# Kernel optimization log

Hardware: AMD Instinct MI355X
Metric: run time of the kernel (lower is better)

## Reference

```python
import jax, jax.numpy as jnp
import numpy as np

N, E, B = 100000, 500000, 64
H, C = 2, 128  # GAT heads, per-head channels
EPS = 1e-5


def _seg_mean(x, idx, n):
    s = jax.ops.segment_sum(x, idx, num_segments=n)
    cnt = jax.ops.segment_sum(jnp.ones((idx.shape[0],), x.dtype), idx, num_segments=n)
    cnt = jnp.maximum(cnt, 1.0)
    return s / cnt.reshape((n,) + (1,) * (x.ndim - 1))


def _bn(x, g, b):
    m = x.mean(0)
    v = x.var(0)  # biased, as torch BN uses for normalization
    return g * (x - m) / jnp.sqrt(v + EPS) + b


def _sage(x, src, dst, n, wl, wr, b):
    # PyG SAGEConv(mean): lin_l(mean_j x_j) + lin_r(x_i), bias on lin_l
    agg = _seg_mean(x[src], dst, n)
    return agg @ wl.T + x @ wr.T + b


def setup_inputs():
    key = jax.random.key(0)
    ks = jax.random.split(key, 24)
    w = lambda k, s: (jax.random.normal(k, s, jnp.float32) * 0.05)
    inp = {
        'pos': jax.random.normal(ks[0], (N, 3), jnp.float32),
        'edge_index': jax.random.randint(ks[1], (2, E), 0, N),
        'batch': jnp.sort(jax.random.randint(ks[2], (N,), 0, B)),
        # SAGEConv 1: 3 -> 128
        's1_wl': w(ks[3], (128, 3)), 's1_wr': w(ks[4], (128, 3)), 's1_b': jnp.zeros((128,), jnp.float32),
        # SAGEConv 2: 128 -> 128
        's2_wl': w(ks[5], (128, 128)), 's2_wr': w(ks[6], (128, 128)), 's2_b': jnp.zeros((128,), jnp.float32),
        # GATConv: 256 -> 128, heads=2, concat=False
        'g_w': w(ks[7], (H * C, 256)), 'g_asrc': w(ks[8], (H, C)), 'g_adst': w(ks[9], (H, C)), 'g_b': jnp.zeros((C,), jnp.float32),
        # decoder
        'd1_w': w(ks[10], (256, 128)), 'd1_b': jnp.zeros((256,), jnp.float32),
        'bn1_g': jnp.ones((256,), jnp.float32), 'bn1_b': jnp.zeros((256,), jnp.float32),
        'd2_w': w(ks[11], (128, 256)), 'd2_b': jnp.zeros((128,), jnp.float32),
        'bn2_g': jnp.ones((128,), jnp.float32), 'bn2_b': jnp.zeros((128,), jnp.float32),
        'd3_w': w(ks[12], (40, 128)), 'd3_b': jnp.zeros((40,), jnp.float32),
        'bn3_g': jnp.ones((40,), jnp.float32), 'bn3_b': jnp.zeros((40,), jnp.float32),
    }
    return inp


def reference(pos, edge_index, batch, s1_wl, s1_wr, s1_b, s2_wl, s2_wr, s2_b,
              g_w, g_asrc, g_adst, g_b, d1_w, d1_b, bn1_g, bn1_b,
              d2_w, d2_b, bn2_g, bn2_b, d3_w, d3_b, bn3_g, bn3_b):
    src, dst = edge_index[0], edge_index[1]

    x1 = jax.nn.relu(_sage(pos, src, dst, N, s1_wl, s1_wr, s1_b))
    x2 = jax.nn.relu(_sage(x1, src, dst, N, s2_wl, s2_wr, s2_b))
    x3 = jnp.concatenate([x1, x2], axis=-1)  # [N, 256]

    # GATConv with self-loops, dropout off (eval), aggr='mean'
    loop = jnp.arange(N, dtype=edge_index.dtype)
    src_sl = jnp.concatenate([src, loop])
    dst_sl = jnp.concatenate([dst, loop])
    xw = (x3 @ g_w.T).reshape(N, H, C)
    a_src = (xw * g_asrc).sum(-1)  # [N, H]
    a_dst = (xw * g_adst).sum(-1)
    e = jax.nn.leaky_relu(a_src[src_sl] + a_dst[dst_sl], 0.2)  # [E+N, H]
    e_max = jax.ops.segment_max(e, dst_sl, num_segments=N)
    e = jnp.exp(e - e_max[dst_sl])
    denom = jax.ops.segment_sum(e, dst_sl, num_segments=N)
    alpha = e / denom[dst_sl]
    msg = alpha[:, :, None] * xw[src_sl]  # [E+N, H, C]
    out = _seg_mean(msg, dst_sl, N)  # aggr='mean' over incoming edges
    x3 = out.mean(axis=1) + g_b  # average heads (concat=False) -> [N, 128]

    z = _seg_mean(x3, batch, B)  # global mean pool -> [B, 128]

    z = jax.nn.relu(_bn(z @ d1_w.T + d1_b, bn1_g, bn1_b))
    z = jax.nn.relu(_bn(z @ d2_w.T + d2_b, bn2_g, bn2_b))
    z = _bn(z @ d3_w.T + d3_b, bn3_g, bn3_b)
    return z, jnp.argmax(z, axis=-1)
```

## Files before the change

kernel.cpp:

```cpp
#include <hip/hip_runtime.h>
#include <math.h>

#define BN_EPS 1e-5f

typedef __attribute__((ext_vector_type(8))) short short8;
typedef __attribute__((ext_vector_type(4))) float f32x4;

__device__ __forceinline__ float bf2f(unsigned short u) {
  return __builtin_bit_cast(float, ((unsigned)u) << 16);
}
__device__ __forceinline__ unsigned short f2bf(float f) {
  unsigned u = __builtin_bit_cast(unsigned, f);
  unsigned r = (u + 0x7fffu + ((u >> 16) & 1u)) >> 16;
  return (unsigned short)r;
}
__device__ __forceinline__ void fsplit(float x, unsigned short& h, unsigned short& l) {
  h = f2bf(x);
  l = f2bf(x - bf2f(h));
}

__global__ void k_deg_sum1(const int* __restrict__ src, const int* __restrict__ dst,
                           const float* __restrict__ pos, int* __restrict__ deg,
                           float* __restrict__ sum1, int E) {
  int e = blockIdx.x * blockDim.x + threadIdx.x;
  if (e >= E) return;
  int s = src[e], d = dst[e];
  atomicAdd(&deg[d], 1);
  atomicAdd(&sum1[d * 3 + 0], pos[s * 3 + 0]);
  atomicAdd(&sum1[d * 3 + 1], pos[s * 3 + 1]);
  atomicAdd(&sum1[d * 3 + 2], pos[s * 3 + 2]);
}

__global__ void k_scan1(const int* __restrict__ deg, int* __restrict__ rowptr,
                        int* __restrict__ bsum, int N) {
  __shared__ int part[256];
  int t = threadIdx.x;
  int base = blockIdx.x * 1024;
  int v[4]; int s = 0;
#pragma unroll
  for (int i = 0; i < 4; i++) {
    int idx = base + t * 4 + i;
    v[i] = (idx < N) ? deg[idx] : 0;
    s += v[i];
  }
  part[t] = s;
  __syncthreads();
  for (int off = 1; off < 256; off <<= 1) {
    int x = (t >= off) ? part[t - off] : 0;
    __syncthreads();
    part[t] += x;
    __syncthreads();
  }
  int run = part[t] - s;
#pragma unroll
  for (int i = 0; i < 4; i++) {
    int idx = base + t * 4 + i;
    if (idx < N) rowptr[idx] = run;
    run += v[i];
  }
  if (t == 255) bsum[blockIdx.x] = part[255];
}

__global__ void k_scan2(int* __restrict__ bsum, int nb) {
  if (threadIdx.x == 0 && blockIdx.x == 0) {
    int run = 0;
    for (int i = 0; i < nb; i++) { int v = bsum[i]; bsum[i] = run; run += v; }
  }
}

__global__ void k_scan3(int* __restrict__ rowptr, const int* __restrict__ bsum,
                        int N, int E) {
  int i = blockIdx.x * blockDim.x + threadIdx.x;
  if (i < N) rowptr[i] += bsum[i >> 10];
  else if (i == N) rowptr[N] = E;
}

__global__ void k_fill(const int* __restrict__ src, const int* __restrict__ dst,
                       const int* __restrict__ rowptr, int* __restrict__ fill,
                       int* __restrict__ col, int E) {
  int e = blockIdx.x * blockDim.x + threadIdx.x;
  if (e >= E) return;
  int d = dst[e];
  int p = rowptr[d] + atomicAdd(&fill[d], 1);
  col[p] = src[e];
}

__global__ void k_sage1(const float* __restrict__ sum1, const int* __restrict__ deg,
                        const float* __restrict__ pos,
                        const float* __restrict__ wl, const float* __restrict__ wr,
                        const float* __restrict__ b,
                        unsigned short* __restrict__ catH, unsigned short* __restrict__ catL,
                        int N) {
  int n = blockIdx.x;
  if (n >= N) return;
  int o = threadIdx.x;
  float c = fmaxf((float)deg[n], 1.f);
  float a0 = sum1[n * 3 + 0] / c, a1 = sum1[n * 3 + 1] / c, a2 = sum1[n * 3 + 2] / c;
  float p0 = pos[n * 3 + 0], p1 = pos[n * 3 + 1], p2 = pos[n * 3 + 2];
  float v = b[o] + wl[o * 3 + 0] * a0 + wl[o * 3 + 1] * a1 + wl[o * 3 + 2] * a2
                 + wr[o * 3 + 0] * p0 + wr[o * 3 + 1] * p1 + wr[o * 3 + 2] * p2;
  v = fmaxf(v, 0.f);
  unsigned short h, l;
  fsplit(v, h, l);
  catH[(size_t)n * 256 + o] = h;
  catL[(size_t)n * 256 + o] = l;
}

__global__ void k_agg_x1(const int* __restrict__ rowptr, const int* __restrict__ col,
                         const unsigned short* __restrict__ catH,
                         const unsigned short* __restrict__ catL,
                         unsigned short* __restrict__ aggH,
                         unsigned short* __restrict__ aggL, int N) {
  int w = (blockIdx.x * blockDim.x + threadIdx.x) >> 6;
  int nw = (gridDim.x * blockDim.x) >> 6;
  int lane = threadIdx.x & 63;
  for (int n = w; n < N; n += nw) {
    int k0 = rowptr[n], k1 = rowptr[n + 1];
    float ax = 0.f, ay = 0.f;
    int k = k0;
    for (; k + 1 < k1; k += 2) {
      int s0 = col[k], s1 = col[k + 1];
      size_t b0 = (size_t)s0 * 256 + lane * 2;
      size_t b1 = (size_t)s1 * 256 + lane * 2;
      ushort2 h0 = *(const ushort2*)&catH[b0];
      ushort2 l0 = *(const ushort2*)&catL[b0];
      ushort2 h1 = *(const ushort2*)&catH[b1];
      ushort2 l1 = *(const ushort2*)&catL[b1];
      ax += (bf2f(h0.x) + bf2f(l0.x)) + (bf2f(h1.x) + bf2f(l1.x));
      ay += (bf2f(h0.y) + bf2f(l0.y)) + (bf2f(h1.y) + bf2f(l1.y));
    }
    if (k < k1) {
      int s = col[k];
      size_t b0 = (size_t)s * 256 + lane * 2;
      ushort2 vh = *(const ushort2*)&catH[b0];
      ushort2 vl = *(const ushort2*)&catL[b0];
      ax += bf2f(vh.x) + bf2f(vl.x);
      ay += bf2f(vh.y) + bf2f(vl.y);
    }
    float inv = 1.f / fmaxf((float)(k1 - k0), 1.f);
    unsigned short hx, lx, hy, ly;
    fsplit(ax * inv, hx, lx);
    fsplit(ay * inv, hy, ly);
    *(ushort2*)&aggH[(size_t)n * 128 + lane * 2] = make_ushort2(hx, hy);
    *(ushort2*)&aggL[(size_t)n * 128 + lane * 2] = make_ushort2(lx, ly);
  }
}

__global__ void k_castcat(const float* __restrict__ a, const float* __restrict__ b,
                          unsigned short* __restrict__ oH, unsigned short* __restrict__ oL,
                          int K1, int K2, int M) {
  int i = blockIdx.x * blockDim.x + threadIdx.x;
  int K = K1 + K2;
  if (i >= M * K) return;
  int m = i / K, k = i - m * K;
  float v = (k < K1) ? a[m * K1 + k] : b[m * K2 + (k - K1)];
  unsigned short h, l;
  fsplit(v, h, l);
  oH[i] = h;
  oL[i] = l;
}

__global__ __launch_bounds__(256) void gemm_split(
    const unsigned short* __restrict__ AH1, const unsigned short* __restrict__ AL1,
    int as1, int K1,
    const unsigned short* __restrict__ AH2, const unsigned short* __restrict__ AL2,
    int as2,
    const unsigned short* __restrict__ WH, const unsigned short* __restrict__ WL,
    const float* __restrict__ bias,
    unsigned short* __restrict__ CH, unsigned short* __restrict__ CL,
    int cs, int co, int Nr, int K, int relu,
    const float* __restrict__ asrc, const float* __restrict__ adst,
    float* __restrict__ attn) {
  __shared__ unsigned short AsH[128][40];
  __shared__ unsigned short AsL[128][40];
  __shared__ unsigned short BsH[128][40];
  __shared__ unsigned short BsL[128][40];
  int tid = threadIdx.x;
  int bm = blockIdx.x, bn = blockIdx.y;
  int wv = tid >> 6, L = tid & 63;
  int m16 = L & 15, quad = L >> 4;
  int rbase = wv * 32;

  f32x4 acc[2][8];
#pragma unroll
  for (int i = 0; i < 2; i++)
#pragma unroll
    for (int j = 0; j < 8; j++) acc[i][j] = (f32x4){0.f, 0.f, 0.f, 0.f};

  for (int kt = 0; kt < K; kt += 32) {
    const unsigned short *ApH, *ApL;
    int ast, kl;
    if (kt < K1) { ApH = AH1; ApL = AL1; ast = as1; kl = kt; }
    else         { ApH = AH2; ApL = AL2; ast = as2; kl = kt - K1; }
#pragma unroll
    for (int i = 0; i < 2; i++) {
      int flat = tid * 2 + i;
      int row = flat >> 2;
      int kc = (flat & 3) * 8;
      int rg = bm * 128 + row;
      uint4 vah = {0u, 0u, 0u, 0u}, val = {0u, 0u, 0u, 0u};
      if (rg < Nr) {
        size_t a = (size_t)rg * ast + kl + kc;
        vah = *(const uint4*)&ApH[a];
        val = *(const uint4*)&ApL[a];
      }
      *(uint4*)&AsH[row][kc] = vah;
      *(uint4*)&AsL[row][kc] = val;
      int ng = bn * 128 + row;
      size_t wb = (size_t)ng * K + kt + kc;
      *(uint4*)&BsH[row][kc] = *(const uint4*)&WH[wb];
      *(uint4*)&BsL[row][kc] = *(const uint4*)&WL[wb];
    }
    __syncthreads();
    short8 afH[2], afL[2];
#pragma unroll
    for (int rt = 0; rt < 2; rt++) {
      afH[rt] = *(const short8*)&AsH[rbase + rt * 16 + m16][quad * 8];
      afL[rt] = *(const short8*)&AsL[rbase + rt * 16 + m16][quad * 8];
    }
#pragma unroll
    for (int ct = 0; ct < 8; ct++) {
      short8 bfH = *(const short8*)&BsH[ct * 16 + m16][quad * 8];
      short8 bfL = *(const short8*)&BsL[ct * 16 + m16][quad * 8];
#pragma unroll
      for (int rt = 0; rt < 2; rt++) {
        acc[rt][ct] = __builtin_amdgcn_mfma_f32_16x16x32_bf16(afH[rt], bfH, acc[rt][ct], 0, 0, 0);
        acc[rt][ct] = __builtin_amdgcn_mfma_f32_16x16x32_bf16(afH[rt], bfL, acc[rt][ct], 0, 0, 0);
        acc[rt][ct] = __builtin_amdgcn_mfma_f32_16x16x32_bf16(afL[rt], bfH, acc[rt][ct], 0, 0, 0);
      }
    }
    __syncthreads();
  }

  const bool doattn = (attn != nullptr);
  float sa[2][4], sd[2][4];
#pragma unroll
  for (int rt = 0; rt < 2; rt++)
#pragma unroll
    for (int r = 0; r < 4; r++) { sa[rt][r] = 0.f; sd[rt][r] = 0.f; }

#pragma unroll
  for (int rt = 0; rt < 2; rt++) {
#pragma unroll
    for (int r = 0; r < 4; r++) {
      int rg = bm * 128 + rbase + rt * 16 + quad * 4 + r;
      if (rg >= Nr) continue;
#pragma unroll
      for (int ct = 0; ct < 8; ct++) {
        int cg = bn * 128 + ct * 16 + m16;
        float v = acc[rt][ct][r];
        if (doattn) {
          sa[rt][r] += v * asrc[cg];
          sd[rt][r] += v * adst[cg];
        }
        if (bias) v += bias[cg];
        if (relu) v = fmaxf(v, 0.f);
        unsigned short h, l;
        fsplit(v, h, l);
        size_t o = (size_t)rg * cs + co + cg;
        CH[o] = h;
        CL[o] = l;
      }
    }
  }

  if (doattn) {
#pragma unroll
    for (int rt = 0; rt < 2; rt++) {
#pragma unroll
      for (int r = 0; r < 4; r++) {
        float a = sa[rt][r], d = sd[rt][r];
#pragma unroll
        for (int m = 8; m >= 1; m >>= 1) {
          a += __shfl_xor(a, m);
          d += __shfl_xor(d, m);
        }
        if (m16 == 0) {
          int rg = bm * 128 + rbase + rt * 16 + quad * 4 + r;
          if (rg < Nr) {
            attn[rg * 4 + bn] = a;
            attn[rg * 4 + 2 + bn] = d;
          }
        }
      }
    }
  }
}

__global__ void k_gat_gather(const int* __restrict__ rowptr, const int* __restrict__ col,
                             const unsigned short* __restrict__ xwH,
                             const unsigned short* __restrict__ xwL,
                             const float* __restrict__ attn,
                             const float* __restrict__ gb, float* __restrict__ x3g, int N) {
  int w = (blockIdx.x * blockDim.x + threadIdx.x) >> 6;
  int nw = (gridDim.x * blockDim.x) >> 6;
  int lane = threadIdx.x & 63;
  int h = lane >> 5;
  for (int n = w; n < N; n += nw) {
    int k0 = rowptr[n], k1 = rowptr[n + 1];
    float ad = attn[n * 4 + 2 + h];
    float a0 = 0.f, a1 = 0.f, a2 = 0.f, a3 = 0.f, den = 0.f;
    int k = k0;
    for (; k + 1 < k1; k += 2) {
      int s0 = col[k], s1 = col[k + 1];
      float e0 = attn[s0 * 4 + h] + ad;
      float e1 = attn[s1 * 4 + h] + ad;
      e0 = e0 >= 0.f ? e0 : 0.2f * e0;
      e1 = e1 >= 0.f ? e1 : 0.2f * e1;
      float w0 = expf(e0), w1 = expf(e1);
      size_t b0 = (size_t)s0 * 256 + lane * 4;
      size_t b1 = (size_t)s1 * 256 + lane * 4;
      ushort4 h0 = *(const ushort4*)&xwH[b0];
      ushort4 l0 = *(const ushort4*)&xwL[b0];
      ushort4 h1 = *(const ushort4*)&xwH[b1];
      ushort4 l1 = *(const ushort4*)&xwL[b1];
      a0 += w0 * (bf2f(h0.x) + bf2f(l0.x)) + w1 * (bf2f(h1.x) + bf2f(l1.x));
      a1 += w0 * (bf2f(h0.y) + bf2f(l0.y)) + w1 * (bf2f(h1.y) + bf2f(l1.y));
      a2 += w0 * (bf2f(h0.z) + bf2f(l0.z)) + w1 * (bf2f(h1.z) + bf2f(l1.z));
      a3 += w0 * (bf2f(h0.w) + bf2f(l0.w)) + w1 * (bf2f(h1.w) + bf2f(l1.w));
      den += w0 + w1;
    }
    if (k < k1) {
      int s = col[k];
      float ea = attn[s * 4 + h] + ad;
      float el = ea >= 0.f ? ea : 0.2f * ea;
      float wgt = expf(el);
      size_t base = (size_t)s * 256 + lane * 4;
      ushort4 xh = *(const ushort4*)&xwH[base];
      ushort4 xl = *(const ushort4*)&xwL[base];
      a0 += wgt * (bf2f(xh.x) + bf2f(xl.x));
      a1 += wgt * (bf2f(xh.y) + bf2f(xl.y));
      a2 += wgt * (bf2f(xh.z) + bf2f(xl.z));
      a3 += wgt * (bf2f(xh.w) + bf2f(xl.w));
      den += wgt;
    }
    {
      float ea = attn[n * 4 + h] + ad;
      float el = ea >= 0.f ? ea : 0.2f * ea;
      float wgt = expf(el);
      size_t base = (size_t)n * 256 + lane * 4;
      ushort4 xh = *(const ushort4*)&xwH[base];
      ushort4 xl = *(const ushort4*)&xwL[base];
      a0 += wgt * (bf2f(xh.x) + bf2f(xl.x));
      a1 += wgt * (bf2f(xh.y) + bf2f(xl.y));
      a2 += wgt * (bf2f(xh.z) + bf2f(xl.z));
      a3 += wgt * (bf2f(xh.w) + bf2f(xl.w));
      den += wgt;
    }
    float invD = 1.f / den;
    float q0 = a0 * invD, q1 = a1 * invD, q2 = a2 * invD, q3 = a3 * invD;
    float p0 = __shfl_xor(q0, 32), p1 = __shfl_xor(q1, 32);
    float p2 = __shfl_xor(q2, 32), p3 = __shfl_xor(q3, 32);
    if (lane < 32) {
      float invc = 1.f / (float)(k1 - k0 + 1);
      float4 g = *(const float4*)&gb[lane * 4];
      float4 r;
      r.x = 0.5f * (q0 + p0) * invc + g.x;
      r.y = 0.5f * (q1 + p1) * invc + g.y;
      r.z = 0.5f * (q2 + p2) * invc + g.z;
      r.w = 0.5f * (q3 + p3) * invc + g.w;
      *(float4*)&x3g[(size_t)n * 128 + lane * 4] = r;
    }
  }
}

__global__ void k_pool(const float* __restrict__ x3g, const int* __restrict__ batch,
                       float* __restrict__ zsum, float* __restrict__ zcnt, int N) {
  int t = threadIdx.x;
  int chunk = (N + gridDim.x - 1) / gridDim.x;
  int n0 = blockIdx.x * chunk;
  int n1 = min(N, n0 + chunk);
  if (n0 >= n1) return;
  int cur = batch[n0];
  float acc = 0.f, cacc = 0.f;
  for (int n = n0; n < n1; n++) {
    int b = batch[n];
    if (b != cur) {
      atomicAdd(&zsum[cur * 128 + t], acc);
      if (t == 0) atomicAdd(&zcnt[cur], cacc);
      acc = 0.f; cacc = 0.f; cur = b;
    }
    acc += x3g[(size_t)n * 128 + t];
    cacc += 1.f;
  }
  atomicAdd(&zsum[cur * 128 + t], acc);
  if (t == 0) atomicAdd(&zcnt[cur], cacc);
}

__global__ void dec_col(const float* __restrict__ X, float* __restrict__ Y,
                        const float* __restrict__ W, const float* __restrict__ bias,
                        const float* __restrict__ g, const float* __restrict__ beta,
                        int Ki, int Mo, int Bn, int relu,
                        const float* __restrict__ zcntp) {
  int m = blockIdx.x;
  int r = threadIdx.x;
  float dot = 0.f;
  const float* xr = &X[(size_t)r * Ki];
  const float* wr = &W[(size_t)m * Ki];
  for (int k = 0; k < Ki; k += 4) {
    float4 xv = *(const float4*)&xr[k];
    float4 wv = *(const float4*)&wr[k];
    dot += xv.x * wv.x + xv.y * wv.y + xv.z * wv.z + xv.w * wv.w;
  }
  if (zcntp) dot *= 1.f / fmaxf(zcntp[r], 1.f);
  float acc = dot + bias[m];
  float s = acc;
#pragma unroll
  for (int o = 32; o >= 1; o >>= 1) s += __shfl_xor(s, o);
  float mean = s / (float)Bn;
  float d = acc - mean;
  float v2 = d * d;
#pragma unroll
  for (int o = 32; o >= 1; o >>= 1) v2 += __shfl_xor(v2, o);
  float var = v2 / (float)Bn;
  float y = g[m] * d / sqrtf(var + BN_EPS) + beta[m];
  if (relu) y = fmaxf(y, 0.f);
  Y[(size_t)r * Mo + m] = y;
}

__global__ void k_argmax(const float* __restrict__ z, float* __restrict__ argout,
                         int Bn, int Mo) {
  int r = blockIdx.x * blockDim.x + threadIdx.x;
  if (r >= Bn) return;
  const float* yr = &z[(size_t)r * Mo];
  float best = yr[0];
  int bi = 0;
  for (int j = 1; j < Mo; j++)
    if (yr[j] > best) { best = yr[j]; bi = j; }
  argout[r] = (float)bi;
}

extern "C" void kernel_launch(void* const* d_in, const int* in_sizes, int n_in,
                              void* d_out, int out_size, void* d_ws, size_t ws_size,
                              hipStream_t stream) {
  const int N = in_sizes[0] / 3;
  const int E = in_sizes[1] / 2;
  const int Bn = out_size / 41;

  const float* pos = (const float*)d_in[0];
  const int* ei = (const int*)d_in[1];
  const int* src = ei;
  const int* dst = ei + E;
  const int* batch = (const int*)d_in[2];
  const float* s1_wl = (const float*)d_in[3];
  const float* s1_wr = (const float*)d_in[4];
  const float* s1_b  = (const float*)d_in[5];
  const float* s2_wl = (const float*)d_in[6];
  const float* s2_wr = (const float*)d_in[7];
  const float* s2_b  = (const float*)d_in[8];
  const float* g_w    = (const float*)d_in[9];
  const float* g_asrc = (const float*)d_in[10];
  const float* g_adst = (const float*)d_in[11];
  const float* g_b    = (const float*)d_in[12];
  const float* d1_w = (const float*)d_in[13];
  const float* d1_b = (const float*)d_in[14];
  const float* bn1_g = (const float*)d_in[15];
  const float* bn1_b = (const float*)d_in[16];
  const float* d2_w = (const float*)d_in[17];
  const float* d2_b = (const float*)d_in[18];
  const float* bn2_g = (const float*)d_in[19];
  const float* bn2_b = (const float*)d_in[20];
  const float* d3_w = (const float*)d_in[21];
  const float* d3_b = (const float*)d_in[22];
  const float* bn3_g = (const float*)d_in[23];
  const float* bn3_b = (const float*)d_in[24];

  size_t Ns = (size_t)N, Es = (size_t)E;
  char* p = (char*)d_ws;
  auto take = [&](size_t bytes) -> char* {
    char* r = p;
    p += (bytes + 255) & ~(size_t)255;
    return r;
  };
  int* deg    = (int*)take(Ns * 4);
  int* fillc  = (int*)take(Ns * 4);
  int* rowptr = (int*)take((Ns + 1) * 4);
  int* bsums  = (int*)take(1024);
  int* col    = (int*)take(Es * 4);
  float* sum1 = (float*)take(3 * Ns * 4);
  float* attn = (float*)take(4 * Ns * 4);
  unsigned short* catH = (unsigned short*)take(256 * Ns * 2);
  unsigned short* catL = (unsigned short*)take(256 * Ns * 2);
  unsigned short* aggH = (unsigned short*)take(128 * Ns * 2);
  unsigned short* aggL = (unsigned short*)take(128 * Ns * 2);
  unsigned short* xwH  = (unsigned short*)take(256 * Ns * 2);
  unsigned short* xwL  = (unsigned short*)take(256 * Ns * 2);
  unsigned short* wcH  = (unsigned short*)take(128 * 256 * 2);
  unsigned short* wcL  = (unsigned short*)take(128 * 256 * 2);
  unsigned short* gwH  = (unsigned short*)take(256 * 256 * 2);
  unsigned short* gwL  = (unsigned short*)take(256 * 256 * 2);
  float* zsum  = (float*)take(8192 * 4);
  float* zcnt  = (float*)take(256 * 4);
  float* db1   = (float*)take(16384 * 4);
  float* db2   = (float*)take(8192 * 4);
  float* x3g = (float*)aggH;
  float* out = (float*)d_out;

  hipMemsetAsync(deg, 0, Ns * 4, stream);
  hipMemsetAsync(fillc, 0, Ns * 4, stream);
  hipMemsetAsync(sum1, 0, 3 * Ns * 4, stream);
  hipMemsetAsync(zsum, 0, 8192 * 4, stream);
  hipMemsetAsync(zcnt, 0, 256 * 4, stream);

  k_deg_sum1<<<(E + 255) / 256, 256, 0, stream>>>(src, dst, pos, deg, sum1, E);

  int nb = (N + 1023) / 1024;
  k_scan1<<<nb, 256, 0, stream>>>(deg, rowptr, bsums, N);
  k_scan2<<<1, 64, 0, stream>>>(bsums, nb);
  k_scan3<<<(N + 256) / 256, 256, 0, stream>>>(rowptr, bsums, N, E);
  k_fill<<<(E + 255) / 256, 256, 0, stream>>>(src, dst, rowptr, fillc, col, E);

  k_castcat<<<(128 * 256 + 255) / 256, 256, 0, stream>>>(s2_wl, s2_wr, wcH, wcL, 128, 128, 128);
  k_castcat<<<(256 * 256 + 255) / 256, 256, 0, stream>>>(g_w, nullptr, gwH, gwL, 256, 0, 256);

  k_sage1<<<N, 128, 0, stream>>>(sum1, deg, pos, s1_wl, s1_wr, s1_b, catH, catL, N);
  k_agg_x1<<<2048, 256, 0, stream>>>(rowptr, col, catH, catL, aggH, aggL, N);

  dim3 g2((N + 127) / 128, 1);
  gemm_split<<<g2, 256, 0, stream>>>(aggH, aggL, 128, 128, catH, catL, 256,
                                     wcH, wcL, s2_b, catH, catL, 256, 128, N, 256, 1,
                                     nullptr, nullptr, nullptr);

  dim3 g3((N + 127) / 128, 2);
  gemm_split<<<g3, 256, 0, stream>>>(catH, catL, 256, 256, nullptr, nullptr, 0,
                                     gwH, gwL, nullptr, xwH, xwL, 256, 0, N, 256, 0,
                                     g_asrc, g_adst, attn);

  k_gat_gather<<<2048, 256, 0, stream>>>(rowptr, col, xwH, xwL, attn, g_b, x3g, N);

  k_pool<<<2048, 128, 0, stream>>>(x3g, batch, zsum, zcnt, N);

  dec_col<<<256, Bn, 0, stream>>>(zsum, db1, d1_w, d1_b, bn1_g, bn1_b, 128, 256, Bn, 1, zcnt);
  dec_col<<<128, Bn, 0, stream>>>(db1, db2, d2_w, d2_b, bn2_g, bn2_b, 256, 128, Bn, 1, nullptr);
  dec_col<<<40, Bn, 0, stream>>>(db2, out, d3_w, d3_b, bn3_g, bn3_b, 128, 40, Bn, 0, nullptr);
  k_argmax<<<1, 64, 0, stream>>>(out, out + Bn * 40, Bn, 40);
}
```

Before: 684.4 us.

## Interleave bf16 hi/lo split into packed words and stage GEMM epilogue through LDS

Activation buffers (cat, agg, xw) switch from separate hi/lo bf16 planes to one array of packed 32-bit words holding both halves. Each gather then does one wider load per row instead of two separate ones. The GEMM epilogue writes its packed results into the shared-memory tile, then stores full rows with coalesced 16-byte writes instead of scattered 2-byte stores, and the GEMM prologue unpacks the interleaved A tile into hi/lo LDS planes. This adds bit-shuffling ALU work and extra syncs in the epilogue.

```diff
diff --git a/kernel.cpp b/kernel.cpp
--- a/kernel.cpp
+++ b/kernel.cpp
@@ -5,6 +5,7 @@
 
 typedef __attribute__((ext_vector_type(8))) short short8;
 typedef __attribute__((ext_vector_type(4))) float f32x4;
+typedef unsigned int uint_t;
 
 __device__ __forceinline__ float bf2f(unsigned short u) {
   return __builtin_bit_cast(float, ((unsigned)u) << 16);
@@ -14,9 +15,13 @@
   unsigned r = (u + 0x7fffu + ((u >> 16) & 1u)) >> 16;
   return (unsigned short)r;
 }
-__device__ __forceinline__ void fsplit(float x, unsigned short& h, unsigned short& l) {
-  h = f2bf(x);
-  l = f2bf(x - bf2f(h));
+__device__ __forceinline__ uint_t packsplit(float x) {
+  unsigned short h = f2bf(x);
+  unsigned short l = f2bf(x - bf2f(h));
+  return (uint_t)h | ((uint_t)l << 16);
+}
+__device__ __forceinline__ float unpk(uint_t u) {
+  return bf2f((unsigned short)(u & 0xffffu)) + bf2f((unsigned short)(u >> 16));
 }
 
 __global__ void k_deg_sum1(const int* __restrict__ src, const int* __restrict__ dst,
@@ -89,8 +94,7 @@
                         const float* __restrict__ pos,
                         const float* __restrict__ wl, const float* __restrict__ wr,
                         const float* __restrict__ b,
-                        unsigned short* __restrict__ catH, unsigned short* __restrict__ catL,
-                        int N) {
+                        uint_t* __restrict__ cat, int N) {
   int n = blockIdx.x;
   if (n >= N) return;
   int o = threadIdx.x;
@@ -99,18 +103,12 @@
   float p0 = pos[n * 3 + 0], p1 = pos[n * 3 + 1], p2 = pos[n * 3 + 2];
   float v = b[o] + wl[o * 3 + 0] * a0 + wl[o * 3 + 1] * a1 + wl[o * 3 + 2] * a2
                  + wr[o * 3 + 0] * p0 + wr[o * 3 + 1] * p1 + wr[o * 3 + 2] * p2;
-  v = fmaxf(v, 0.f);
-  unsigned short h, l;
-  fsplit(v, h, l);
-  catH[(size_t)n * 256 + o] = h;
-  catL[(size_t)n * 256 + o] = l;
+  cat[(size_t)n * 256 + o] = packsplit(fmaxf(v, 0.f));
 }
 
 __global__ void k_agg_x1(const int* __restrict__ rowptr, const int* __restrict__ col,
-                         const unsigned short* __restrict__ catH,
-                         const unsigned short* __restrict__ catL,
-                         unsigned short* __restrict__ aggH,
-                         unsigned short* __restrict__ aggL, int N) {
+                         const uint_t* __restrict__ cat,
+                         uint_t* __restrict__ agg, int N) {
   int w = (blockIdx.x * blockDim.x + threadIdx.x) >> 6;
   int nw = (gridDim.x * blockDim.x) >> 6;
   int lane = threadIdx.x & 63;
@@ -120,29 +118,22 @@
     int k = k0;
     for (; k + 1 < k1; k += 2) {
       int s0 = col[k], s1 = col[k + 1];
-      size_t b0 = (size_t)s0 * 256 + lane * 2;
-      size_t b1 = (size_t)s1 * 256 + lane * 2;
-      ushort2 h0 = *(const ushort2*)&catH[b0];
-      ushort2 l0 = *(const ushort2*)&catL[b0];
-      ushort2 h1 = *(const ushort2*)&catH[b1];
-      ushort2 l1 = *(const ushort2*)&catL[b1];
-      ax += (bf2f(h0.x) + bf2f(l0.x)) + (bf2f(h1.x) + bf2f(l1.x));
-      ay += (bf2f(h0.y) + bf2f(l0.y)) + (bf2f(h1.y) + bf2f(l1.y));
+      uint2 v0 = *(const uint2*)&cat[(size_t)s0 * 256 + lane * 2];
+      uint2 v1 = *(const uint2*)&cat[(size_t)s1 * 256 + lane * 2];
+      ax += unpk(v0.x) + unpk(v1.x);
+      ay += unpk(v0.y) + unpk(v1.y);
     }
     if (k < k1) {
       int s = col[k];
-      size_t b0 = (size_t)s * 256 + lane * 2;
-      ushort2 vh = *(const ushort2*)&catH[b0];
-      ushort2 vl = *(const ushort2*)&catL[b0];
-      ax += bf2f(vh.x) + bf2f(vl.x);
-      ay += bf2f(vh.y) + bf2f(vl.y);
+      uint2 v = *(const uint2*)&cat[(size_t)s * 256 + lane * 2];
+      ax += unpk(v.x);
+      ay += unpk(v.y);
     }
     float inv = 1.f / fmaxf((float)(k1 - k0), 1.f);
-    unsigned short hx, lx, hy, ly;
-    fsplit(ax * inv, hx, lx);
-    fsplit(ay * inv, hy, ly);
-    *(ushort2*)&aggH[(size_t)n * 128 + lane * 2] = make_ushort2(hx, hy);
-    *(ushort2*)&aggL[(size_t)n * 128 + lane * 2] = make_ushort2(lx, ly);
+    uint2 o;
+    o.x = packsplit(ax * inv);
+    o.y = packsplit(ay * inv);
+    *(uint2*)&agg[(size_t)n * 128 + lane * 2] = o;
   }
 }
 
@@ -154,27 +145,24 @@
   if (i >= M * K) return;
   int m = i / K, k = i - m * K;
   float v = (k < K1) ? a[m * K1 + k] : b[m * K2 + (k - K1)];
-  unsigned short h, l;
-  fsplit(v, h, l);
+  unsigned short h = f2bf(v);
   oH[i] = h;
-  oL[i] = l;
+  oL[i] = f2bf(v - bf2f(h));
 }
 
 __global__ __launch_bounds__(256) void gemm_split(
-    const unsigned short* __restrict__ AH1, const unsigned short* __restrict__ AL1,
-    int as1, int K1,
-    const unsigned short* __restrict__ AH2, const unsigned short* __restrict__ AL2,
-    int as2,
+    const uint_t* __restrict__ A1, int as1, int K1,
+    const uint_t* __restrict__ A2, int as2,
     const unsigned short* __restrict__ WH, const unsigned short* __restrict__ WL,
     const float* __restrict__ bias,
-    unsigned short* __restrict__ CH, unsigned short* __restrict__ CL,
-    int cs, int co, int Nr, int K, int relu,
+    uint_t* __restrict__ C, int cs, int co, int Nr, int K, int relu,
     const float* __restrict__ asrc, const float* __restrict__ adst,
     float* __restrict__ attn) {
-  __shared__ unsigned short AsH[128][40];
-  __shared__ unsigned short AsL[128][40];
-  __shared__ unsigned short BsH[128][40];
-  __shared__ unsigned short BsL[128][40];
+  __shared__ unsigned short smem[4 * 128 * 40];
+  unsigned short (*AsH)[40] = (unsigned short (*)[40])smem;
+  unsigned short (*AsL)[40] = (unsigned short (*)[40])(smem + 128 * 40);
+  unsigned short (*BsH)[40] = (unsigned short (*)[40])(smem + 2 * 128 * 40);
+  unsigned short (*BsL)[40] = (unsigned short (*)[40])(smem + 3 * 128 * 40);
   int tid = threadIdx.x;
   int bm = blockIdx.x, bn = blockIdx.y;
   int wv = tid >> 6, L = tid & 63;
@@ -188,24 +176,28 @@
     for (int j = 0; j < 8; j++) acc[i][j] = (f32x4){0.f, 0.f, 0.f, 0.f};
 
   for (int kt = 0; kt < K; kt += 32) {
-    const unsigned short *ApH, *ApL;
+    const uint_t* Ap;
     int ast, kl;
-    if (kt < K1) { ApH = AH1; ApL = AL1; ast = as1; kl = kt; }
-    else         { ApH = AH2; ApL = AL2; ast = as2; kl = kt - K1; }
+    if (kt < K1) { Ap = A1; ast = as1; kl = kt; }
+    else         { Ap = A2; ast = as2; kl = kt - K1; }
 #pragma unroll
     for (int i = 0; i < 2; i++) {
       int flat = tid * 2 + i;
       int row = flat >> 2;
       int kc = (flat & 3) * 8;
       int rg = bm * 128 + row;
-      uint4 vah = {0u, 0u, 0u, 0u}, val = {0u, 0u, 0u, 0u};
+      uint4 p0 = {0u, 0u, 0u, 0u}, p1 = {0u, 0u, 0u, 0u};
       if (rg < Nr) {
-        size_t a = (size_t)rg * ast + kl + kc;
-        vah = *(const uint4*)&ApH[a];
-        val = *(const uint4*)&ApL[a];
+        const uint_t* ap = &Ap[(size_t)rg * ast + kl + kc];
+        p0 = *(const uint4*)ap;
+        p1 = *(const uint4*)(ap + 4);
       }
-      *(uint4*)&AsH[row][kc] = vah;
-      *(uint4*)&AsL[row][kc] = val;
+      uint_t h0 = (p0.x & 0xffffu) | (p0.y << 16), l0 = (p0.x >> 16) | (p0.y & 0xffff0000u);
+      uint_t h1 = (p0.z & 0xffffu) | (p0.w << 16), l1 = (p0.z >> 16) | (p0.w & 0xffff0000u);
+      uint_t h2 = (p1.x & 0xffffu) | (p1.y << 16), l2 = (p1.x >> 16) | (p1.y & 0xffff0000u);
+      uint_t h3 = (p1.z & 0xffffu) | (p1.w << 16), l3 = (p1.z >> 16) | (p1.w & 0xffff0000u);
+      *(uint4*)&AsH[row][kc] = make_uint4(h0, h1, h2, h3);
+      *(uint4*)&AsL[row][kc] = make_uint4(l0, l1, l2, l3);
       int ng = bn * 128 + row;
       size_t wb = (size_t)ng * K + kt + kc;
       *(uint4*)&BsH[row][kc] = *(const uint4*)&WH[wb];
@@ -232,44 +224,19 @@
     __syncthreads();
   }
 
-  const bool doattn = (attn != nullptr);
-  float sa[2][4], sd[2][4];
-#pragma unroll
-  for (int rt = 0; rt < 2; rt++)
-#pragma unroll
-    for (int r = 0; r < 4; r++) { sa[rt][r] = 0.f; sd[rt][r] = 0.f; }
-
-#pragma unroll
-  for (int rt = 0; rt < 2; rt++) {
-#pragma unroll
-    for (int r = 0; r < 4; r++) {
-      int rg = bm * 128 + rbase + rt * 16 + quad * 4 + r;
-      if (rg >= Nr) continue;
-#pragma unroll
-      for (int ct = 0; ct < 8; ct++) {
-        int cg = bn * 128 + ct * 16 + m16;
-        float v = acc[rt][ct][r];
-        if (doattn) {
-          sa[rt][r] += v * asrc[cg];
-          sd[rt][r] += v * adst[cg];
+  if (attn) {
+#pragma unroll
+    for (int rt = 0; rt < 2; rt++) {
+#pragma unroll
+      for (int r = 0; r < 4; r++) {
+        float a = 0.f, d = 0.f;
+#pragma unroll
+        for (int ct = 0; ct < 8; ct++) {
+          int cg = bn * 128 + ct * 16 + m16;
+          float v = acc[rt][ct][r];
+          a += v * asrc[cg];
+          d += v * adst[cg];
         }
-        if (bias) v += bias[cg];
-        if (relu) v = fmaxf(v, 0.f);
-        unsigned short h, l;
-        fsplit(v, h, l);
-        size_t o = (size_t)rg * cs + co + cg;
-        CH[o] = h;
-        CL[o] = l;
-      }
-    }
-  }
-
-  if (doattn) {
-#pragma unroll
-    for (int rt = 0; rt < 2; rt++) {
-#pragma unroll
-      for (int r = 0; r < 4; r++) {
-        float a = sa[rt][r], d = sd[rt][r];
 #pragma unroll
         for (int m = 8; m >= 1; m >>= 1) {
           a += __shfl_xor(a, m);
@@ -285,11 +252,44 @@
       }
     }
   }
+
+  uint_t* T = (uint_t*)smem;
+#pragma unroll
+  for (int hc = 0; hc < 2; hc++) {
+    if (hc) __syncthreads();
+#pragma unroll
+    for (int rt = 0; rt < 2; rt++) {
+#pragma unroll
+      for (int ctl = 0; ctl < 4; ctl++) {
+        int ct = hc * 4 + ctl;
+        int cg = bn * 128 + ct * 16 + m16;
+        float bco = bias ? bias[cg] : 0.f;
+#pragma unroll
+        for (int r = 0; r < 4; r++) {
+          int row = rbase + rt * 16 + quad * 4 + r;
+          float v = acc[rt][ct][r] + bco;
+          if (relu) v = fmaxf(v, 0.f);
+          T[row * 65 + ctl * 16 + m16] = packsplit(v);
+        }
+      }
+    }
+    __syncthreads();
+    int row = tid >> 1;
+    int cb = (tid & 1) * 32;
+    int rg = bm * 128 + row;
+    if (rg < Nr) {
+      size_t base = (size_t)rg * cs + co + bn * 128 + hc * 64 + cb;
+#pragma unroll
+      for (int i2 = 0; i2 < 8; i2++) {
+        uint4 q = *(const uint4*)&T[row * 65 + cb + i2 * 4];
+        *(uint4*)&C[base + i2 * 4] = q;
+      }
+    }
+  }
 }
 
 __global__ void k_gat_gather(const int* __restrict__ rowptr, const int* __restrict__ col,
-                             const unsigned short* __restrict__ xwH,
-                             const unsigned short* __restrict__ xwL,
+                             const uint_t* __restrict__ xw,
                              const float* __restrict__ attn,
                              const float* __restrict__ gb, float* __restrict__ x3g, int N) {
   int w = (blockIdx.x * blockDim.x + threadIdx.x) >> 6;
@@ -308,16 +308,12 @@
       e0 = e0 >= 0.f ? e0 : 0.2f * e0;
       e1 = e1 >= 0.f ? e1 : 0.2f * e1;
       float w0 = expf(e0), w1 = expf(e1);
-      size_t b0 = (size_t)s0 * 256 + lane * 4;
-      size_t b1 = (size_t)s1 * 256 + lane * 4;
-      ushort4 h0 = *(const ushort4*)&xwH[b0];
-      ushort4 l0 = *(const ushort4*)&xwL[b0];
-      ushort4 h1 = *(const ushort4*)&xwH[b1];
-      ushort4 l1 = *(const ushort4*)&xwL[b1];
-      a0 += w0 * (bf2f(h0.x) + bf2f(l0.x)) + w1 * (bf2f(h1.x) + bf2f(l1.x));
-      a1 += w0 * (bf2f(h0.y) + bf2f(l0.y)) + w1 * (bf2f(h1.y) + bf2f(l1.y));
-      a2 += w0 * (bf2f(h0.z) + bf2f(l0.z)) + w1 * (bf2f(h1.z) + bf2f(l1.z));
-      a3 += w0 * (bf2f(h0.w) + bf2f(l0.w)) + w1 * (bf2f(h1.w) + bf2f(l1.w));
+      uint4 x0 = *(const uint4*)&xw[(size_t)s0 * 256 + lane * 4];
+      uint4 x1 = *(const uint4*)&xw[(size_t)s1 * 256 + lane * 4];
+      a0 += w0 * unpk(x0.x) + w1 * unpk(x1.x);
+      a1 += w0 * unpk(x0.y) + w1 * unpk(x1.y);
+      a2 += w0 * unpk(x0.z) + w1 * unpk(x1.z);
+      a3 += w0 * unpk(x0.w) + w1 * unpk(x1.w);
       den += w0 + w1;
     }
     if (k < k1) {
@@ -325,26 +321,18 @@
       float ea = attn[s * 4 + h] + ad;
       float el = ea >= 0.f ? ea : 0.2f * ea;
       float wgt = expf(el);
-      size_t base = (size_t)s * 256 + lane * 4;
-      ushort4 xh = *(const ushort4*)&xwH[base];
-      ushort4 xl = *(const ushort4*)&xwL[base];
-      a0 += wgt * (bf2f(xh.x) + bf2f(xl.x));
-      a1 += wgt * (bf2f(xh.y) + bf2f(xl.y));
-      a2 += wgt * (bf2f(xh.z) + bf2f(xl.z));
-      a3 += wgt * (bf2f(xh.w) + bf2f(xl.w));
+      uint4 x = *(const uint4*)&xw[(size_t)s * 256 + lane * 4];
+      a0 += wgt * unpk(x.x); a1 += wgt * unpk(x.y);
+      a2 += wgt * unpk(x.z); a3 += wgt * unpk(x.w);
       den += wgt;
     }
     {
       float ea = attn[n * 4 + h] + ad;
       float el = ea >= 0.f ? ea : 0.2f * ea;
       float wgt = expf(el);
-      size_t base = (size_t)n * 256 + lane * 4;
-      ushort4 xh = *(const ushort4*)&xwH[base];
-      ushort4 xl = *(const ushort4*)&xwL[base];
-      a0 += wgt * (bf2f(xh.x) + bf2f(xl.x));
-      a1 += wgt * (bf2f(xh.y) + bf2f(xl.y));
-      a2 += wgt * (bf2f(xh.z) + bf2f(xl.z));
-      a3 += wgt * (bf2f(xh.w) + bf2f(xl.w));
+      uint4 x = *(const uint4*)&xw[(size_t)n * 256 + lane * 4];
+      a0 += wgt * unpk(x.x); a1 += wgt * unpk(x.y);
+      a2 += wgt * unpk(x.z); a3 += wgt * unpk(x.w);
       den += wgt;
     }
     float invD = 1.f / den;
@@ -479,21 +467,18 @@
   int* col    = (int*)take(Es * 4);
   float* sum1 = (float*)take(3 * Ns * 4);
   float* attn = (float*)take(4 * Ns * 4);
-  unsigned short* catH = (unsigned short*)take(256 * Ns * 2);
-  unsigned short* catL = (unsigned short*)take(256 * Ns * 2);
-  unsigned short* aggH = (unsigned short*)take(128 * Ns * 2);
-  unsigned short* aggL = (unsigned short*)take(128 * Ns * 2);
-  unsigned short* xwH  = (unsigned short*)take(256 * Ns * 2);
-  unsigned short* xwL  = (unsigned short*)take(256 * Ns * 2);
-  unsigned short* wcH  = (unsigned short*)take(128 * 256 * 2);
-  unsigned short* wcL  = (unsigned short*)take(128 * 256 * 2);
-  unsigned short* gwH  = (unsigned short*)take(256 * 256 * 2);
-  unsigned short* gwL  = (unsigned short*)take(256 * 256 * 2);
+  uint_t* cat = (uint_t*)take(256 * Ns * 4);
+  uint_t* agg = (uint_t*)take(128 * Ns * 4);
+  uint_t* xw  = (uint_t*)take(256 * Ns * 4);
+  unsigned short* wcH = (unsigned short*)take(128 * 256 * 2);
+  unsigned short* wcL = (unsigned short*)take(128 * 256 * 2);
+  unsigned short* gwH = (unsigned short*)take(256 * 256 * 2);
+  unsigned short* gwL = (unsigned short*)take(256 * 256 * 2);
   float* zsum  = (float*)take(8192 * 4);
   float* zcnt  = (float*)take(256 * 4);
   float* db1   = (float*)take(16384 * 4);
   float* db2   = (float*)take(8192 * 4);
-  float* x3g = (float*)aggH;
+  float* x3g = (float*)agg;
   float* out = (float*)d_out;
 
   hipMemsetAsync(deg, 0, Ns * 4, stream);
@@ -513,20 +498,20 @@
   k_castcat<<<(128 * 256 + 255) / 256, 256, 0, stream>>>(s2_wl, s2_wr, wcH, wcL, 128, 128, 128);
   k_castcat<<<(256 * 256 + 255) / 256, 256, 0, stream>>>(g_w, nullptr, gwH, gwL, 256, 0, 256);
 
-  k_sage1<<<N, 128, 0, stream>>>(sum1, deg, pos, s1_wl, s1_wr, s1_b, catH, catL, N);
-  k_agg_x1<<<2048, 256, 0, stream>>>(rowptr, col, catH, catL, aggH, aggL, N);
+  k_sage1<<<N, 128, 0, stream>>>(sum1, deg, pos, s1_wl, s1_wr, s1_b, cat, N);
+  k_agg_x1<<<2048, 256, 0, stream>>>(rowptr, col, cat, agg, N);
 
   dim3 g2((N + 127) / 128, 1);
-  gemm_split<<<g2, 256, 0, stream>>>(aggH, aggL, 128, 128, catH, catL, 256,
-                                     wcH, wcL, s2_b, catH, catL, 256, 128, N, 256, 1,
+  gemm_split<<<g2, 256, 0, stream>>>(agg, 128, 128, cat, 256,
+                                     wcH, wcL, s2_b, cat, 256, 128, N, 256, 1,
                                      nullptr, nullptr, nullptr);
 
   dim3 g3((N + 127) / 128, 2);
-  gemm_split<<<g3, 256, 0, stream>>>(catH, catL, 256, 256, nullptr, nullptr, 0,
-                                     gwH, gwL, nullptr, xwH, xwL, 256, 0, N, 256, 0,
+  gemm_split<<<g3, 256, 0, stream>>>(cat, 256, 256, nullptr, 0,
+                                     gwH, gwL, nullptr, xw, 256, 0, N, 256, 0,
                                      g_asrc, g_adst, attn);
 
-  k_gat_gather<<<2048, 256, 0, stream>>>(rowptr, col, xwH, xwL, attn, g_b, x3g, N);
+  k_gat_gather<<<2048, 256, 0, stream>>>(rowptr, col, xw, attn, g_b, x3g, N);
 
   k_pool<<<2048, 128, 0, stream>>>(x3g, batch, zsum, zcnt, N);
 
```

Measured after the change: 639.8 us. -6.5%, faster.
